# Kernel tuning notes

Hardware: AMD Instinct MI355X
Metric: run time of the kernel (lower is better)

## Reference

```python
import jax, jax.numpy as jnp
import numpy as np

EPS = 0.1           # entropic regularization epsilon
MAX_ITER = 100
THRESH = 0.1        # early-stop threshold on mean |u - u_prev|
LOG_EPS = 1e-8


def setup_inputs() -> dict:
    key = jax.random.key(0)
    kx, ky = jax.random.split(key)
    x = jax.random.normal(kx, (8, 1024, 3), dtype=jnp.float32)
    y = jax.random.normal(ky, (8, 1024, 3), dtype=jnp.float32)
    return {"x": x, "y": y}


def _sqdist(x, y):
    # squared euclidean cost matrix [B, N, N]  (== torch.cdist(x,y,p=2)**2)
    x2 = jnp.sum(x * x, axis=-1)[:, :, None]
    y2 = jnp.sum(y * y, axis=-1)[:, None, :]
    xy = jnp.einsum("bnd,bmd->bnm", x, y)
    return jnp.maximum(x2 + y2 - 2.0 * xy, 0.0)


def reference(x, y):
    B, N, D = x.shape
    C = _sqdist(x, y)                      # [B, N, N]
    log_mu = jnp.log(1.0 / N + LOG_EPS)    # scalar (uniform marginals)
    log_nu = log_mu

    u0 = jnp.zeros((B, N), dtype=x.dtype)
    v0 = jnp.zeros((B, N), dtype=x.dtype)

    def step(carry, _):
        u, v, done = carry
        # u-update uses old v
        M1 = (u[:, :, None] + v[:, None, :] - C) / EPS          # [B,N,N]
        u_new = EPS * (log_mu - jax.nn.logsumexp(M1, axis=-1)) + u
        # v-update uses new u
        M2 = (u_new[:, :, None] + v[:, None, :] - C) / EPS
        v_new = EPS * (log_nu - jax.nn.logsumexp(M2, axis=-2)) + v
        # freeze once converged (mimics torch early break)
        u_out = jnp.where(done, u, u_new)
        v_out = jnp.where(done, v, v_new)
        err = jnp.mean(jnp.abs(u_out - u))
        done_new = done | (err < THRESH)
        return (u_out, v_out, done_new), None

    (u, v, _), _ = jax.lax.scan(step, (u0, v0, jnp.array(False)), None, length=MAX_ITER)

    PI = jnp.exp((u[:, :, None] + v[:, None, :] - C) / EPS)     # transport plan
    emd = jnp.sum(PI * C, axis=(-2, -1))                        # [B]
    return jnp.mean(emd)                                        # reduction='mean'
```

## Files before the change

### kernel.cpp

```cpp
#include <hip/hip_runtime.h>

typedef unsigned int uint_t;

constexpr int B = 8;
constexpr int N = 1024;
constexpr int NBLOCKS = 256;
constexpr int NTHREADS = 512;
constexpr int NWAVES = NTHREADS / 64;
constexpr int BPB = NBLOCKS / B;
constexpr int SEG = N / BPB;
constexpr int RPW = SEG / NWAVES;
constexpr int KPL = N / 64;
constexpr int MAX_ITER = 100;
constexpr float THRESH = 0.1f;
constexpr float K2 = 14.42695040888963f;
constexpr float A2K = 2.0f * K2;
constexpr float NEPSLN2 = -0.06931471805599453f;
constexpr float EPSLOGMU = -0.693146156565634f;
constexpr uint_t MAGIC = 0xC0FFEE01u;

constexpr int OFF_U      = 0;
constexpr int OFF_V      = OFF_U + B * N;
constexpr int OFF_ERRBLK = OFF_V + B * N;
constexpr int OFF_ERRBAT = OFF_ERRBLK + 256;
constexpr int OFF_EMDBLK = OFF_ERRBAT + 800;
constexpr int OFF_EMDBAT = OFF_EMDBLK + 256;
constexpr int OFF_ZERO   = OFF_EMDBAT + 8;
constexpr int OFF_ERRPUB = OFF_ZERO;
constexpr int OFF_EMDPUB = OFF_ERRPUB + 100;
constexpr int OFF_BARCNT = ((OFF_EMDPUB + 1 + 31) / 32) * 32;
constexpr int OFF_ZEROEND= OFF_BARCNT + 8 * 32;
constexpr int OFF_INIT   = OFF_ZEROEND;

__device__ __forceinline__ float gload(const float* p) {
  return __hip_atomic_load(p, __ATOMIC_RELAXED, __HIP_MEMORY_SCOPE_AGENT);
}
__device__ __forceinline__ void gstore(float* p, float v) {
  __hip_atomic_store(p, v, __ATOMIC_RELAXED, __HIP_MEMORY_SCOPE_AGENT);
}

__device__ __forceinline__ float wsum(float v) {
#pragma unroll
  for (int o = 32; o; o >>= 1) v += __shfl_xor(v, o);
  return v;
}
__device__ __forceinline__ float wmax(float v) {
#pragma unroll
  for (int o = 32; o; o >>= 1) v = fmaxf(v, __shfl_xor(v, o));
  return v;
}

__device__ __forceinline__ float block_sum(float v, float* sh) {
  v = wsum(v);
  const int wave = threadIdx.x >> 6;
  const int lane = threadIdx.x & 63;
  if (lane == 0) sh[wave] = v;
  __syncthreads();
  float tot = 0.f;
#pragma unroll
  for (int w = 0; w < NWAVES; ++w) tot += sh[w];
  __syncthreads();
  return tot;
}

__device__ __forceinline__ void batch_barrier(uint_t* cnt, uint_t target) {
  __syncthreads();
  if (threadIdx.x == 0) {
    __hip_atomic_fetch_add(cnt, 1u, __ATOMIC_RELEASE, __HIP_MEMORY_SCOPE_AGENT);
    while (__hip_atomic_load(cnt, __ATOMIC_RELAXED, __HIP_MEMORY_SCOPE_AGENT) < target)
      __builtin_amdgcn_s_sleep(1);
  }
  __syncthreads();
}

template <bool TRACK>
__device__ __forceinline__ float half_update(
    const float4* s_row, const float4* s_col,
    const float* __restrict__ pin, float* __restrict__ pout,
    int seg, int wave, int lane, bool pin_zero, bool first_out) {
  float p2[KPL];
#pragma unroll
  for (int k = 0; k < KPL; ++k)
    p2[k] = pin_zero ? 0.f : gload(&pin[lane + (k << 6)]) * K2;

  float err = 0.f;
  float a0[RPW], a1[RPW], a2[RPW], X[RPW], m[RPW];
  float vals[RPW][KPL];
#pragma unroll
  for (int rr = 0; rr < RPW; ++rr) {
    float4 r4 = s_row[seg * SEG + wave * RPW + rr];
    a0[rr] = A2K * r4.x; a1[rr] = A2K * r4.y; a2[rr] = A2K * r4.z;
    X[rr] = -r4.w;
    m[rr] = -3.4e38f;
  }
#pragma unroll
  for (int k = 0; k < KPL; ++k) {
    float4 c4 = s_col[lane + (k << 6)];
    float pv = p2[k];
#pragma unroll
    for (int rr = 0; rr < RPW; ++rr) {
      float t = fmaf(a0[rr], c4.x, fmaf(a1[rr], c4.y, fmaf(a2[rr], c4.z, c4.w)));
      float val = fminf(t - X[rr], 0.f) + pv;
      vals[rr][k] = val;
      m[rr] = fmaxf(m[rr], val);
    }
  }
#pragma unroll
  for (int rr = 0; rr < RPW; ++rr) {
    float mr = wmax(m[rr]);
    float s = 0.f;
#pragma unroll
    for (int k = 0; k < KPL; ++k)
      s += __builtin_amdgcn_exp2f(vals[rr][k] - mr);
    s = wsum(s);
    float lse2 = mr + __builtin_amdgcn_logf(s);
    float pnew = fmaf(NEPSLN2, lse2, EPSLOGMU);
    if (lane == 0) {
      int i = seg * SEG + wave * RPW + rr;
      if (TRACK) {
        float old = first_out ? 0.f : gload(&pout[i]);
        err += fabsf(pnew - old);
      }
      gstore(&pout[i], pnew);
    }
  }
  return err;
}

__global__ void __launch_bounds__(NTHREADS, 1) sinkhorn_kernel(
    const float* __restrict__ xg, const float* __restrict__ yg,
    float* __restrict__ out, float* __restrict__ ws) {
  __shared__ float4 s_x4[N];
  __shared__ float4 s_y4[N];
  __shared__ float sh_red[NWAVES];

  const int bid = blockIdx.x;
  const int tid = threadIdx.x;
  const int b = bid & 7;
  const int seg = bid >> 3;
  const int wave = tid >> 6;
  const int lane = tid & 63;

  float* u = ws + OFF_U + b * N;
  float* v = ws + OFF_V + b * N;
  float* err_blk = ws + OFF_ERRBLK + b * 32;
  float* err_bat = ws + OFF_ERRBAT;
  float* emd_blk = ws + OFF_EMDBLK + b * 32;
  float* emd_bat = ws + OFF_EMDBAT;
  uint_t* err_pub = (uint_t*)(ws + OFF_ERRPUB);
  uint_t* emd_pub = (uint_t*)(ws + OFF_EMDPUB);
  uint_t* init_flag = (uint_t*)(ws + OFF_INIT);
  uint_t* bar_cnt = (uint_t*)(ws + OFF_BARCNT) + b * 32;

  for (int p = tid; p < N; p += NTHREADS) {
    const float* xp = xg + (size_t)(b * N + p) * 3;
    float x0 = xp[0], x1 = xp[1], x2 = xp[2];
    s_x4[p] = make_float4(x0, x1, x2, -K2 * (x0 * x0 + x1 * x1 + x2 * x2));
    const float* yp = yg + (size_t)(b * N + p) * 3;
    float y0 = yp[0], y1 = yp[1], y2 = yp[2];
    s_y4[p] = make_float4(y0, y1, y2, -K2 * (y0 * y0 + y1 * y1 + y2 * y2));
  }

  if (bid == 0) {
    uint_t* zb = (uint_t*)(ws + OFF_ZERO);
    for (int i = tid; i < OFF_ZEROEND - OFF_ZERO; i += NTHREADS)
      __hip_atomic_store(&zb[i], 0u, __ATOMIC_RELAXED, __HIP_MEMORY_SCOPE_AGENT);
    __syncthreads();
    if (tid == 0)
      __hip_atomic_store(init_flag, MAGIC, __ATOMIC_RELEASE, __HIP_MEMORY_SCOPE_AGENT);
  } else if (tid == 0) {
    while (__hip_atomic_load(init_flag, __ATOMIC_RELAXED, __HIP_MEMORY_SCOPE_AGENT) != MAGIC)
      __builtin_amdgcn_s_sleep(2);
  }
  __syncthreads();

  uint_t bar_target = 0;
  for (int it = 0; it < MAX_ITER; ++it) {
    float my_err = half_update<true>(s_x4, s_y4, v, u, seg, wave, lane,
                                     it == 0, it == 0);
    float blk_err = block_sum(my_err, sh_red);
    if (tid == 0) gstore(&err_blk[seg], blk_err);
    bar_target += BPB;
    batch_barrier(bar_cnt, bar_target);

    if (seg == 0 && tid == 0) {
      float s = 0.f;
      for (int q = 0; q < BPB; ++q) s += gload(&err_blk[q]);
      gstore(&err_bat[it * B + b], s);
      __hip_atomic_fetch_add(&err_pub[it], 1u, __ATOMIC_RELEASE, __HIP_MEMORY_SCOPE_AGENT);
    }

    half_update<false>(s_y4, s_x4, u, v, seg, wave, lane, false, false);
    bar_target += BPB;
    batch_barrier(bar_cnt, bar_target);

    if (tid == 0)
      while (__hip_atomic_load(&err_pub[it], __ATOMIC_RELAXED, __HIP_MEMORY_SCOPE_AGENT) < (uint_t)B)
        __builtin_amdgcn_s_sleep(2);
    __syncthreads();
    float tot = 0.f;
#pragma unroll
    for (int q = 0; q < B; ++q) tot += gload(&err_bat[it * B + q]);
    if (tot * (1.f / (B * N)) < THRESH) break;
  }

  float p2[KPL];
#pragma unroll
  for (int k = 0; k < KPL; ++k) p2[k] = gload(&v[lane + (k << 6)]) * K2;
  float acc = 0.f;
#pragma unroll
  for (int rr = 0; rr < RPW; ++rr) {
    int i = seg * SEG + wave * RPW + rr;
    float4 r4 = s_x4[i];
    float a0 = A2K * r4.x, a1 = A2K * r4.y, a2 = A2K * r4.z;
    float X = -r4.w;
    float u2 = gload(&u[i]) * K2;
#pragma unroll
    for (int k = 0; k < KPL; ++k) {
      float4 c4 = s_y4[lane + (k << 6)];
      float t = fmaf(a0, c4.x, fmaf(a1, c4.y, fmaf(a2, c4.z, c4.w)));
      float kc = fmaxf(X - t, 0.f);
      acc = fmaf(__builtin_amdgcn_exp2f(u2 + p2[k] - kc), kc, acc);
    }
  }
  float blk = block_sum(acc, sh_red);
  if (tid == 0) gstore(&emd_blk[seg], blk);
  bar_target += BPB;
  batch_barrier(bar_cnt, bar_target);
  if (seg == 0 && tid == 0) {
    float s = 0.f;
    for (int q = 0; q < BPB; ++q) s += gload(&emd_blk[q]);
    gstore(&emd_bat[b], s);
    __hip_atomic_fetch_add(emd_pub, 1u, __ATOMIC_RELEASE, __HIP_MEMORY_SCOPE_AGENT);
  }
  if (bid == 0 && tid == 0) {
    while (__hip_atomic_load(emd_pub, __ATOMIC_RELAXED, __HIP_MEMORY_SCOPE_AGENT) < (uint_t)B)
      __builtin_amdgcn_s_sleep(2);
    float s = 0.f;
#pragma unroll
    for (int q = 0; q < B; ++q) s += gload(&emd_bat[q]);
    out[0] = s * (1.f / (B * K2));
  }
}

extern "C" void kernel_launch(void* const* d_in, const int* in_sizes, int n_in,
                              void* d_out, int out_size, void* d_ws, size_t ws_size,
                              hipStream_t stream) {
  const float* x = (const float*)d_in[0];
  const float* y = (const float*)d_in[1];
  float* out = (float*)d_out;
  float* ws = (float*)d_ws;
  void* args[] = { (void*)&x, (void*)&y, (void*)&out, (void*)&ws };
  hipLaunchCooperativeKernel((const void*)sinkhorn_kernel,
                             dim3(NBLOCKS), dim3(NTHREADS), args, 0, stream);
}
```

Baseline: 124.4 us.

## Replace counter barriers with per-block epoch flags and cache columns in registers

Swaps the atomic fetch-add counter barrier for per-block epoch flags that one wave polls in parallel with a wave vote. The per-iteration error and final EMD reductions are likewise gathered by one wave. Column point data for both directions is loaded once into registers instead of being re-read from LDS on every half-update. Rows are now processed one at a time to save registers, and launch bounds ask for 2 blocks per CU. This adds register pressure from holding cX/cY (32 float4 per thread), which may cause spills.

```diff
diff --git a/kernel.cpp b/kernel.cpp
--- a/kernel.cpp
+++ b/kernel.cpp
@@ -26,10 +26,10 @@
 constexpr int OFF_EMDBLK = OFF_ERRBAT + 800;
 constexpr int OFF_EMDBAT = OFF_EMDBLK + 256;
 constexpr int OFF_ZERO   = OFF_EMDBAT + 8;
-constexpr int OFF_ERRPUB = OFF_ZERO;
-constexpr int OFF_EMDPUB = OFF_ERRPUB + 100;
-constexpr int OFF_BARCNT = ((OFF_EMDPUB + 1 + 31) / 32) * 32;
-constexpr int OFF_ZEROEND= OFF_BARCNT + 8 * 32;
+constexpr int OFF_BARFLG = OFF_ZERO;
+constexpr int OFF_ERRFLG = OFF_BARFLG + 256;
+constexpr int OFF_EMDFLG = OFF_ERRFLG + 8;
+constexpr int OFF_ZEROEND= OFF_EMDFLG + 8;
 constexpr int OFF_INIT   = OFF_ZEROEND;
 
 __device__ __forceinline__ float gload(const float* p) {
@@ -37,6 +37,12 @@
 }
 __device__ __forceinline__ void gstore(float* p, float v) {
   __hip_atomic_store(p, v, __ATOMIC_RELAXED, __HIP_MEMORY_SCOPE_AGENT);
+}
+__device__ __forceinline__ uint_t lflag(const uint_t* p) {
+  return __hip_atomic_load(p, __ATOMIC_RELAXED, __HIP_MEMORY_SCOPE_AGENT);
+}
+__device__ __forceinline__ void sflag_rel(uint_t* p, uint_t v) {
+  __hip_atomic_store(p, v, __ATOMIC_RELEASE, __HIP_MEMORY_SCOPE_AGENT);
 }
 
 __device__ __forceinline__ float wsum(float v) {
@@ -63,19 +69,23 @@
   return tot;
 }
 
-__device__ __forceinline__ void batch_barrier(uint_t* cnt, uint_t target) {
-  __syncthreads();
-  if (threadIdx.x == 0) {
-    __hip_atomic_fetch_add(cnt, 1u, __ATOMIC_RELEASE, __HIP_MEMORY_SCOPE_AGENT);
-    while (__hip_atomic_load(cnt, __ATOMIC_RELAXED, __HIP_MEMORY_SCOPE_AGENT) < target)
+__device__ __forceinline__ void batch_barrier(uint_t* flg, int seg, uint_t epoch,
+                                              int lane) {
+  __syncthreads();
+  if (threadIdx.x == 0) sflag_rel(&flg[seg], epoch);
+  if (threadIdx.x < 64) {
+    for (;;) {
+      uint_t f = (lane < BPB) ? lflag(&flg[lane]) : epoch;
+      if (__all(f >= epoch)) break;
       __builtin_amdgcn_s_sleep(1);
+    }
   }
   __syncthreads();
 }
 
 template <bool TRACK>
 __device__ __forceinline__ float half_update(
-    const float4* s_row, const float4* s_col,
+    const float4 (&c)[KPL], const float4* __restrict__ s_row,
     const float* __restrict__ pin, float* __restrict__ pout,
     int seg, int wave, int lane, bool pin_zero, bool first_out) {
   float p2[KPL];
@@ -84,50 +94,37 @@
     p2[k] = pin_zero ? 0.f : gload(&pin[lane + (k << 6)]) * K2;
 
   float err = 0.f;
-  float a0[RPW], a1[RPW], a2[RPW], X[RPW], m[RPW];
-  float vals[RPW][KPL];
 #pragma unroll
   for (int rr = 0; rr < RPW; ++rr) {
-    float4 r4 = s_row[seg * SEG + wave * RPW + rr];
-    a0[rr] = A2K * r4.x; a1[rr] = A2K * r4.y; a2[rr] = A2K * r4.z;
-    X[rr] = -r4.w;
-    m[rr] = -3.4e38f;
-  }
-#pragma unroll
-  for (int k = 0; k < KPL; ++k) {
-    float4 c4 = s_col[lane + (k << 6)];
-    float pv = p2[k];
-#pragma unroll
-    for (int rr = 0; rr < RPW; ++rr) {
-      float t = fmaf(a0[rr], c4.x, fmaf(a1[rr], c4.y, fmaf(a2[rr], c4.z, c4.w)));
-      float val = fminf(t - X[rr], 0.f) + pv;
-      vals[rr][k] = val;
-      m[rr] = fmaxf(m[rr], val);
-    }
-  }
-#pragma unroll
-  for (int rr = 0; rr < RPW; ++rr) {
-    float mr = wmax(m[rr]);
+    const int i = seg * SEG + wave * RPW + rr;
+    float4 r4 = s_row[i];
+    float a0 = A2K * r4.x, a1 = A2K * r4.y, a2 = A2K * r4.z;
+    float X = -r4.w;
+    float vals[KPL];
+    float m = -3.4e38f;
+#pragma unroll
+    for (int k = 0; k < KPL; ++k) {
+      float t = fmaf(a0, c[k].x, fmaf(a1, c[k].y, fmaf(a2, c[k].z, c[k].w)));
+      float val = fminf(t - X, 0.f) + p2[k];
+      vals[k] = val;
+      m = fmaxf(m, val);
+    }
+    m = wmax(m);
     float s = 0.f;
 #pragma unroll
     for (int k = 0; k < KPL; ++k)
-      s += __builtin_amdgcn_exp2f(vals[rr][k] - mr);
+      s += __builtin_amdgcn_exp2f(vals[k] - m);
     s = wsum(s);
-    float lse2 = mr + __builtin_amdgcn_logf(s);
-    float pnew = fmaf(NEPSLN2, lse2, EPSLOGMU);
+    float pnew = fmaf(NEPSLN2, m + __builtin_amdgcn_logf(s), EPSLOGMU);
     if (lane == 0) {
-      int i = seg * SEG + wave * RPW + rr;
-      if (TRACK) {
-        float old = first_out ? 0.f : gload(&pout[i]);
-        err += fabsf(pnew - old);
-      }
+      if (TRACK) err += fabsf(pnew - (first_out ? 0.f : gload(&pout[i])));
       gstore(&pout[i], pnew);
     }
   }
   return err;
 }
 
-__global__ void __launch_bounds__(NTHREADS, 1) sinkhorn_kernel(
+__global__ void __launch_bounds__(NTHREADS, 2) sinkhorn_kernel(
     const float* __restrict__ xg, const float* __restrict__ yg,
     float* __restrict__ out, float* __restrict__ ws) {
   __shared__ float4 s_x4[N];
@@ -147,10 +144,10 @@
   float* err_bat = ws + OFF_ERRBAT;
   float* emd_blk = ws + OFF_EMDBLK + b * 32;
   float* emd_bat = ws + OFF_EMDBAT;
-  uint_t* err_pub = (uint_t*)(ws + OFF_ERRPUB);
-  uint_t* emd_pub = (uint_t*)(ws + OFF_EMDPUB);
+  uint_t* bar_flg = (uint_t*)(ws + OFF_BARFLG) + b * 32;
+  uint_t* err_flg = (uint_t*)(ws + OFF_ERRFLG);
+  uint_t* emd_flg = (uint_t*)(ws + OFF_EMDFLG);
   uint_t* init_flag = (uint_t*)(ws + OFF_INIT);
-  uint_t* bar_cnt = (uint_t*)(ws + OFF_BARCNT) + b * 32;
 
   for (int p = tid; p < N; p += NTHREADS) {
     const float* xp = xg + (size_t)(b * N + p) * 3;
@@ -160,47 +157,60 @@
     float y0 = yp[0], y1 = yp[1], y2 = yp[2];
     s_y4[p] = make_float4(y0, y1, y2, -K2 * (y0 * y0 + y1 * y1 + y2 * y2));
   }
+  __syncthreads();
+
+  float4 cY[KPL], cX[KPL];
+#pragma unroll
+  for (int k = 0; k < KPL; ++k) {
+    cY[k] = s_y4[lane + (k << 6)];
+    cX[k] = s_x4[lane + (k << 6)];
+  }
 
   if (bid == 0) {
     uint_t* zb = (uint_t*)(ws + OFF_ZERO);
     for (int i = tid; i < OFF_ZEROEND - OFF_ZERO; i += NTHREADS)
       __hip_atomic_store(&zb[i], 0u, __ATOMIC_RELAXED, __HIP_MEMORY_SCOPE_AGENT);
     __syncthreads();
-    if (tid == 0)
-      __hip_atomic_store(init_flag, MAGIC, __ATOMIC_RELEASE, __HIP_MEMORY_SCOPE_AGENT);
+    if (tid == 0) sflag_rel(init_flag, MAGIC);
   } else if (tid == 0) {
-    while (__hip_atomic_load(init_flag, __ATOMIC_RELAXED, __HIP_MEMORY_SCOPE_AGENT) != MAGIC)
-      __builtin_amdgcn_s_sleep(2);
-  }
-  __syncthreads();
-
-  uint_t bar_target = 0;
+    while (lflag(init_flag) != MAGIC) __builtin_amdgcn_s_sleep(2);
+  }
+  __syncthreads();
+
+  uint_t epoch = 0;
   for (int it = 0; it < MAX_ITER; ++it) {
-    float my_err = half_update<true>(s_x4, s_y4, v, u, seg, wave, lane,
+    float my_err = half_update<true>(cY, s_x4, v, u, seg, wave, lane,
                                      it == 0, it == 0);
     float blk_err = block_sum(my_err, sh_red);
     if (tid == 0) gstore(&err_blk[seg], blk_err);
-    bar_target += BPB;
-    batch_barrier(bar_cnt, bar_target);
+    ++epoch;
+    batch_barrier(bar_flg, seg, epoch, lane);
 
     if (seg == 0 && tid == 0) {
       float s = 0.f;
       for (int q = 0; q < BPB; ++q) s += gload(&err_blk[q]);
       gstore(&err_bat[it * B + b], s);
-      __hip_atomic_fetch_add(&err_pub[it], 1u, __ATOMIC_RELEASE, __HIP_MEMORY_SCOPE_AGENT);
-    }
-
-    half_update<false>(s_y4, s_x4, u, v, seg, wave, lane, false, false);
-    bar_target += BPB;
-    batch_barrier(bar_cnt, bar_target);
-
-    if (tid == 0)
-      while (__hip_atomic_load(&err_pub[it], __ATOMIC_RELAXED, __HIP_MEMORY_SCOPE_AGENT) < (uint_t)B)
-        __builtin_amdgcn_s_sleep(2);
+      sflag_rel(&err_flg[b], (uint_t)(it + 1));
+    }
+
+    half_update<false>(cX, s_y4, u, v, seg, wave, lane, false, false);
+    ++epoch;
+    batch_barrier(bar_flg, seg, epoch, lane);
+
+    if (tid < 64) {
+      const uint_t want = (uint_t)(it + 1);
+      for (;;) {
+        uint_t f = (lane < B) ? lflag(&err_flg[lane]) : want;
+        if (__all(f >= want)) break;
+        __builtin_amdgcn_s_sleep(1);
+      }
+      float e = (lane < B) ? gload(&err_bat[it * B + lane]) : 0.f;
+      e = wsum(e);
+      if (lane == 0) sh_red[0] = e;
+    }
     __syncthreads();
-    float tot = 0.f;
-#pragma unroll
-    for (int q = 0; q < B; ++q) tot += gload(&err_bat[it * B + q]);
+    float tot = sh_red[0];
+    __syncthreads();
     if (tot * (1.f / (B * N)) < THRESH) break;
   }
 
@@ -210,36 +220,37 @@
   float acc = 0.f;
 #pragma unroll
   for (int rr = 0; rr < RPW; ++rr) {
-    int i = seg * SEG + wave * RPW + rr;
+    const int i = seg * SEG + wave * RPW + rr;
     float4 r4 = s_x4[i];
     float a0 = A2K * r4.x, a1 = A2K * r4.y, a2 = A2K * r4.z;
     float X = -r4.w;
     float u2 = gload(&u[i]) * K2;
 #pragma unroll
     for (int k = 0; k < KPL; ++k) {
-      float4 c4 = s_y4[lane + (k << 6)];
-      float t = fmaf(a0, c4.x, fmaf(a1, c4.y, fmaf(a2, c4.z, c4.w)));
+      float t = fmaf(a0, cY[k].x, fmaf(a1, cY[k].y, fmaf(a2, cY[k].z, cY[k].w)));
       float kc = fmaxf(X - t, 0.f);
       acc = fmaf(__builtin_amdgcn_exp2f(u2 + p2[k] - kc), kc, acc);
     }
   }
   float blk = block_sum(acc, sh_red);
   if (tid == 0) gstore(&emd_blk[seg], blk);
-  bar_target += BPB;
-  batch_barrier(bar_cnt, bar_target);
+  ++epoch;
+  batch_barrier(bar_flg, seg, epoch, lane);
   if (seg == 0 && tid == 0) {
     float s = 0.f;
     for (int q = 0; q < BPB; ++q) s += gload(&emd_blk[q]);
     gstore(&emd_bat[b], s);
-    __hip_atomic_fetch_add(emd_pub, 1u, __ATOMIC_RELEASE, __HIP_MEMORY_SCOPE_AGENT);
-  }
-  if (bid == 0 && tid == 0) {
-    while (__hip_atomic_load(emd_pub, __ATOMIC_RELAXED, __HIP_MEMORY_SCOPE_AGENT) < (uint_t)B)
-      __builtin_amdgcn_s_sleep(2);
-    float s = 0.f;
-#pragma unroll
-    for (int q = 0; q < B; ++q) s += gload(&emd_bat[q]);
-    out[0] = s * (1.f / (B * K2));
+    sflag_rel(&emd_flg[b], 1u);
+  }
+  if (bid == 0 && tid < 64) {
+    for (;;) {
+      uint_t f = (lane < B) ? lflag(&emd_flg[lane]) : 1u;
+      if (__all(f >= 1u)) break;
+      __builtin_amdgcn_s_sleep(1);
+    }
+    float e = (lane < B) ? gload(&emd_bat[lane]) : 0.f;
+    e = wsum(e);
+    if (lane == 0) out[0] = e * (1.f / (B * K2));
   }
 }
 
```

Result: slower. 133.3 us (+7.1%).
